# Performance work log

Hardware: AMD Instinct MI355X
Metric: run time of the kernel (lower is better)

## Reference

```python
import jax, jax.numpy as jnp
import numpy as np

N = 1_000_000
W = 20  # layer_width


def setup_inputs() -> dict:
    key = jax.random.key(0)
    ks = jax.random.split(key, 8)
    s = 0.5  # modest init scale for tanh net
    return {
        "t": jax.random.normal(ks[0], (N, 1), dtype=jnp.float32),
        "W1": jax.random.normal(ks[1], (1, W), dtype=jnp.float32) * s,
        "b1": jnp.zeros((W,), jnp.float32),
        "W2": jax.random.normal(ks[2], (W, W), dtype=jnp.float32) * s / np.sqrt(W),
        "b2": jnp.zeros((W,), jnp.float32),
        "W3": jax.random.normal(ks[3], (W, W), dtype=jnp.float32) * s / np.sqrt(W),
        "b3": jnp.zeros((W,), jnp.float32),
        "W4": jax.random.normal(ks[4], (W, W), dtype=jnp.float32) * s / np.sqrt(W),
        "b4": jnp.zeros((W,), jnp.float32),
        "Wo": jax.random.normal(ks[5], (W, 3), dtype=jnp.float32) * s / np.sqrt(W),
        "bo": jnp.zeros((3,), jnp.float32),
        "c1": jnp.float32(1.0),
        "c2": jnpp if False else jnp.float32(1.0),
        "c3": jnp.float32(1.0),
    }


def reference(t, W1, b1, W2, b2, W3, b3, W4, b4, Wo, bo, c1, c2, c3):
    # DenseBlock(4, 20): four tanh hidden layers + linear head to [x, y, z]
    def mlp(tt):
        h = jnp.tanh(tt @ W1 + b1)
        h = jnp.tanh(h @ W2 + b2)
        h = jnp.tanh(h @ W3 + b3)
        h = jnp.tanh(h @ W4 + b4)
        return h @ Wo + bo  # [N, 3]

    # forward-mode AD: one JVP pass gives d[x,y,z]/dt for every sample
    out, dout = jax.jvp(mlp, (t,), (jnp.ones_like(t),))
    x, y, z = out[:, 0:1], out[:, 1:2], out[:, 2:3]
    dx, dy, dz = dout[:, 0:1], dout[:, 1:2], dout[:, 2:3]
    # Lorenz residuals (log_opt=False -> vars used directly)
    fx = dx - c1 * (y - x)
    fy = dy - x * (c2 - z) + y
    fz = dz - x * y + c3 * z
    return jnp.concatenate([x, y, z, fx, fy, fz], axis=1)  # [N, 6]
```

## Files before the change

kernel.cpp:

```cpp
#include <hip/hip_runtime.h>

#define NBLK 256

__device__ __forceinline__ float fast_tanh(float x) {
    float e = __expf(2.0f * x);
    return 1.0f - 2.0f * __builtin_amdgcn_rcpf(e + 1.0f);
}

__global__ __launch_bounds__(NBLK) void pinn_kernel(
    const float* __restrict__ T,
    const float* __restrict__ W1, const float* __restrict__ b1,
    const float* __restrict__ W2, const float* __restrict__ b2,
    const float* __restrict__ W3, const float* __restrict__ b3,
    const float* __restrict__ W4, const float* __restrict__ b4,
    const float* __restrict__ Wo, const float* __restrict__ bo,
    const float* __restrict__ C1, const float* __restrict__ C2, const float* __restrict__ C3,
    float* __restrict__ out, int n)
{
    __shared__ __align__(16) float sW[1200];
    __shared__ __align__(16) float sB[64];
    __shared__ __align__(16) float sW1[20];
    __shared__ __align__(16) float sb1[20];
    __shared__ __align__(16) float sWoT[64];
    __shared__ float sbo[4];

    const int tid = threadIdx.x;
    for (int i2 = tid; i2 < 400; i2 += NBLK) {
        sW[i2]       = W2[i2];
        sW[400 + i2] = W3[i2];
        sW[800 + i2] = W4[i2];
    }
    if (tid < 20) {
        sW1[tid] = W1[tid];
        sb1[tid] = b1[tid];
        sB[tid]      = b2[tid];
        sB[20 + tid] = b3[tid];
        sB[40 + tid] = b4[tid];
    }
    if (tid < 60) sWoT[(tid % 3) * 20 + (tid / 3)] = Wo[tid];
    if (tid < 3)  sbo[tid] = bo[tid];
    __syncthreads();

    const int i = blockIdx.x * NBLK + tid;
    if (i >= n) return;

    const float t = T[i];

    float h[20], dh[20];

#pragma unroll
    for (int j = 0; j < 20; j += 4) {
        const float4 w = *reinterpret_cast<const float4*>(sW1 + j);
        const float4 b = *reinterpret_cast<const float4*>(sb1 + j);
        float zz[4] = { t * w.x + b.x, t * w.y + b.y, t * w.z + b.z, t * w.w + b.w };
        float dz[4] = { w.x, w.y, w.z, w.w };
#pragma unroll
        for (int q = 0; q < 4; ++q) {
            float e = fast_tanh(zz[q]);
            h[j + q]  = e;
            dh[j + q] = (1.0f - e * e) * dz[q];
        }
    }

#pragma unroll 1
    for (int L = 0; L < 3; ++L) {
        const float* __restrict__ w  = sW + L * 400;
        const float* __restrict__ bb = sB + L * 20;
        float nh[20], ndh[20];
#pragma unroll
        for (int j = 0; j < 20; j += 4) {
            float a0 = bb[j], a1 = bb[j + 1], a2 = bb[j + 2], a3 = bb[j + 3];
            float d0 = 0.f, d1 = 0.f, d2 = 0.f, d3 = 0.f;
#pragma unroll
            for (int k = 0; k < 20; ++k) {
                const float4 ww = *reinterpret_cast<const float4*>(w + k * 20 + j);
                const float hk = h[k], dk = dh[k];
                a0 += hk * ww.x; a1 += hk * ww.y; a2 += hk * ww.z; a3 += hk * ww.w;
                d0 += dk * ww.x; d1 += dk * ww.y; d2 += dk * ww.z; d3 += dk * ww.w;
            }
            float e0 = fast_tanh(a0), e1 = fast_tanh(a1), e2 = fast_tanh(a2), e3 = fast_tanh(a3);
            nh[j] = e0; nh[j + 1] = e1; nh[j + 2] = e2; nh[j + 3] = e3;
            ndh[j]     = (1.0f - e0 * e0) * d0;
            ndh[j + 1] = (1.0f - e1 * e1) * d1;
            ndh[j + 2] = (1.0f - e2 * e2) * d2;
            ndh[j + 3] = (1.0f - e3 * e3) * d3;
        }
#pragma unroll
        for (int j = 0; j < 20; ++j) { h[j] = nh[j]; dh[j] = ndh[j]; }
    }

    float o[3], dO[3];
#pragma unroll
    for (int j = 0; j < 3; ++j) {
        float a = sbo[j], d = 0.f;
#pragma unroll
        for (int k = 0; k < 20; k += 4) {
            const float4 ww = *reinterpret_cast<const float4*>(sWoT + j * 20 + k);
            a += h[k] * ww.x + h[k + 1] * ww.y + h[k + 2] * ww.z + h[k + 3] * ww.w;
            d += dh[k] * ww.x + dh[k + 1] * ww.y + dh[k + 2] * ww.z + dh[k + 3] * ww.w;
        }
        o[j] = a; dO[j] = d;
    }

    const float x = o[0], y = o[1], zz = o[2];
    const float dx = dO[0], dy = dO[1], dz = dO[2];
    const float c1 = C1[0], c2 = C2[0], c3 = C3[0];

    const float fx = dx - c1 * (y - x);
    const float fy = dy - x * (c2 - zz) + y;
    const float fz = dz - x * y + c3 * zz;

    float2* po = reinterpret_cast<float2*>(out + (size_t)i * 6);
    po[0] = make_float2(x,  y);
    po[1] = make_float2(zz, fx);
    po[2] = make_float2(fy, fz);
}

extern "C" void kernel_launch(void* const* d_in, const int* in_sizes, int n_in,
                              void* d_out, int out_size, void* d_ws, size_t ws_size,
                              hipStream_t stream) {
    const float* T  = (const float*)d_in[0];
    const float* W1 = (const float*)d_in[1];
    const float* b1 = (const float*)d_in[2];
    const float* W2 = (const float*)d_in[3];
    const float* b2 = (const float*)d_in[4];
    const float* W3 = (const float*)d_in[5];
    const float* b3 = (const float*)d_in[6];
    const float* W4 = (const float*)d_in[7];
    const float* b4 = (const float*)d_in[8];
    const float* Wo = (const float*)d_in[9];
    const float* bo = (const float*)d_in[10];
    const float* C1 = (const float*)d_in[11];
    const float* C2 = (const float*)d_in[12];
    const float* C3 = (const float*)d_in[13];
    float* out = (float*)d_out;

    const int n = in_sizes[0];
    const int blocks = (n + NBLK - 1) / NBLK;
    pinn_kernel<<<blocks, NBLK, 0, stream>>>(T, W1, b1, W2, b2, W3, b3, W4, b4,
                                             Wo, bo, C1, C2, C3, out, n);
}
```

Before: 178.7 us.

## Read weights directly from global memory as scalar loads and fully unroll layers

Removes the per-block shared-memory staging of weights and the __syncthreads barrier. Weights are now read straight from global memory with uniform addresses, which the compiler can turn into scalar (SMEM) loads held in SGPRs. All three hidden layers are fully unrolled via an inline helper. tanh now uses exp2 with a folded constant. The trade-offs are much larger code size and higher SGPR pressure, possibly with some scalar-load latency, in exchange for dropping LDS traffic and block setup.

```diff
diff --git a/kernel.cpp b/kernel.cpp
--- a/kernel.cpp
+++ b/kernel.cpp
@@ -3,8 +3,32 @@
 #define NBLK 256
 
 __device__ __forceinline__ float fast_tanh(float x) {
-    float e = __expf(2.0f * x);
+    float e = __builtin_amdgcn_exp2f(x * 2.885390082f);
     return 1.0f - 2.0f * __builtin_amdgcn_rcpf(e + 1.0f);
+}
+
+__device__ __forceinline__ void layer(const float* __restrict__ W,
+                                      const float* __restrict__ b,
+                                      float (&h)[20], float (&dh)[20]) {
+    float a[20], d[20];
+#pragma unroll
+    for (int j = 0; j < 20; ++j) { a[j] = b[j]; d[j] = 0.0f; }
+#pragma unroll
+    for (int k = 0; k < 20; ++k) {
+        const float hk = h[k], dk = dh[k];
+#pragma unroll
+        for (int j = 0; j < 20; ++j) {
+            const float w = W[k * 20 + j];
+            a[j] += hk * w;
+            d[j] += dk * w;
+        }
+    }
+#pragma unroll
+    for (int j = 0; j < 20; ++j) {
+        const float e = fast_tanh(a[j]);
+        h[j]  = e;
+        dh[j] = (1.0f - e * e) * d[j];
+    }
 }
 
 __global__ __launch_bounds__(NBLK) void pinn_kernel(
@@ -17,31 +41,7 @@
     const float* __restrict__ C1, const float* __restrict__ C2, const float* __restrict__ C3,
     float* __restrict__ out, int n)
 {
-    __shared__ __align__(16) float sW[1200];
-    __shared__ __align__(16) float sB[64];
-    __shared__ __align__(16) float sW1[20];
-    __shared__ __align__(16) float sb1[20];
-    __shared__ __align__(16) float sWoT[64];
-    __shared__ float sbo[4];
-
-    const int tid = threadIdx.x;
-    for (int i2 = tid; i2 < 400; i2 += NBLK) {
-        sW[i2]       = W2[i2];
-        sW[400 + i2] = W3[i2];
-        sW[800 + i2] = W4[i2];
-    }
-    if (tid < 20) {
-        sW1[tid] = W1[tid];
-        sb1[tid] = b1[tid];
-        sB[tid]      = b2[tid];
-        sB[20 + tid] = b3[tid];
-        sB[40 + tid] = b4[tid];
-    }
-    if (tid < 60) sWoT[(tid % 3) * 20 + (tid / 3)] = Wo[tid];
-    if (tid < 3)  sbo[tid] = bo[tid];
-    __syncthreads();
-
-    const int i = blockIdx.x * NBLK + tid;
+    const int i = blockIdx.x * NBLK + threadIdx.x;
     if (i >= n) return;
 
     const float t = T[i];
@@ -49,66 +49,33 @@
     float h[20], dh[20];
 
 #pragma unroll
-    for (int j = 0; j < 20; j += 4) {
-        const float4 w = *reinterpret_cast<const float4*>(sW1 + j);
-        const float4 b = *reinterpret_cast<const float4*>(sb1 + j);
-        float zz[4] = { t * w.x + b.x, t * w.y + b.y, t * w.z + b.z, t * w.w + b.w };
-        float dz[4] = { w.x, w.y, w.z, w.w };
-#pragma unroll
-        for (int q = 0; q < 4; ++q) {
-            float e = fast_tanh(zz[q]);
-            h[j + q]  = e;
-            dh[j + q] = (1.0f - e * e) * dz[q];
-        }
+    for (int j = 0; j < 20; ++j) {
+        const float w = W1[j];
+        const float e = fast_tanh(t * w + b1[j]);
+        h[j]  = e;
+        dh[j] = (1.0f - e * e) * w;
     }
 
-#pragma unroll 1
-    for (int L = 0; L < 3; ++L) {
-        const float* __restrict__ w  = sW + L * 400;
-        const float* __restrict__ bb = sB + L * 20;
-        float nh[20], ndh[20];
+    layer(W2, b2, h, dh);
+    layer(W3, b3, h, dh);
+    layer(W4, b4, h, dh);
+
+    float o0 = bo[0], o1 = bo[1], o2 = bo[2];
+    float q0 = 0.f,   q1 = 0.f,   q2 = 0.f;
 #pragma unroll
-        for (int j = 0; j < 20; j += 4) {
-            float a0 = bb[j], a1 = bb[j + 1], a2 = bb[j + 2], a3 = bb[j + 3];
-            float d0 = 0.f, d1 = 0.f, d2 = 0.f, d3 = 0.f;
-#pragma unroll
-            for (int k = 0; k < 20; ++k) {
-                const float4 ww = *reinterpret_cast<const float4*>(w + k * 20 + j);
-                const float hk = h[k], dk = dh[k];
-                a0 += hk * ww.x; a1 += hk * ww.y; a2 += hk * ww.z; a3 += hk * ww.w;
-                d0 += dk * ww.x; d1 += dk * ww.y; d2 += dk * ww.z; d3 += dk * ww.w;
-            }
-            float e0 = fast_tanh(a0), e1 = fast_tanh(a1), e2 = fast_tanh(a2), e3 = fast_tanh(a3);
-            nh[j] = e0; nh[j + 1] = e1; nh[j + 2] = e2; nh[j + 3] = e3;
-            ndh[j]     = (1.0f - e0 * e0) * d0;
-            ndh[j + 1] = (1.0f - e1 * e1) * d1;
-            ndh[j + 2] = (1.0f - e2 * e2) * d2;
-            ndh[j + 3] = (1.0f - e3 * e3) * d3;
-        }
-#pragma unroll
-        for (int j = 0; j < 20; ++j) { h[j] = nh[j]; dh[j] = ndh[j]; }
+    for (int k = 0; k < 20; ++k) {
+        const float w0 = Wo[k * 3 + 0], w1 = Wo[k * 3 + 1], w2 = Wo[k * 3 + 2];
+        const float hk = h[k], dk = dh[k];
+        o0 += hk * w0; o1 += hk * w1; o2 += hk * w2;
+        q0 += dk * w0; q1 += dk * w1; q2 += dk * w2;
     }
 
-    float o[3], dO[3];
-#pragma unroll
-    for (int j = 0; j < 3; ++j) {
-        float a = sbo[j], d = 0.f;
-#pragma unroll
-        for (int k = 0; k < 20; k += 4) {
-            const float4 ww = *reinterpret_cast<const float4*>(sWoT + j * 20 + k);
-            a += h[k] * ww.x + h[k + 1] * ww.y + h[k + 2] * ww.z + h[k + 3] * ww.w;
-            d += dh[k] * ww.x + dh[k + 1] * ww.y + dh[k + 2] * ww.z + dh[k + 3] * ww.w;
-        }
-        o[j] = a; dO[j] = d;
-    }
-
-    const float x = o[0], y = o[1], zz = o[2];
-    const float dx = dO[0], dy = dO[1], dz = dO[2];
+    const float x = o0, y = o1, zz = o2;
     const float c1 = C1[0], c2 = C2[0], c3 = C3[0];
 
-    const float fx = dx - c1 * (y - x);
-    const float fy = dy - x * (c2 - zz) + y;
-    const float fz = dz - x * y + c3 * zz;
+    const float fx = q0 - c1 * (y - x);
+    const float fy = q1 - x * (c2 - zz) + y;
+    const float fz = q2 - x * y + c3 * zz;
 
     float2* po = reinterpret_cast<float2*>(out + (size_t)i * 6);
     po[0] = make_float2(x,  y);
```

After: 192.6 us. +7.8%, slower.
